# Performance work log

Hardware: AMD Instinct MI355X
Metric: run time of the kernel (lower is better)

Reference implementation:

```python
import jax, jax.numpy as jnp
import numpy as np

ALPHA = 0.71  # nms_policy.ALPHA: geometric size-bin ratio of HNMS


def _hnms_keep(rects, scores, num):
    """Hashing-based NMS: box survives iff it is the highest-scoring box in its
    hash cell in ALL `num` shifted hash tables. rects is [N,4] cxywh."""
    cx, cy, w, h = rects[:, 0], rects[:, 1], rects[:, 2], rects[:, 3]
    log_a = jnp.log(jnp.asarray(ALPHA, rects.dtype))
    step = 1.0 / ALPHA - 1.0  # location cell size relative to quantized box size
    keep = jnp.ones(scores.shape[0], dtype=bool)
    for m in range(num):  # small fixed number of hash tables
        off = m / num  # fractional shift of each hash table
        # geometric size quantization (w in [1,100], alpha<1 -> qw in [-13,0])
        qw = jnp.floor(jnp.log(w) / log_a + off).astype(jnp.int32)
        qh = jnp.floor(jnp.log(h) / log_a + off).astype(jnp.int32)
        dw = jnp.power(jnp.asarray(ALPHA, rects.dtype), qw.astype(rects.dtype))
        dh = jnp.power(jnp.asarray(ALPHA, rects.dtype), qh.astype(rects.dtype))
        # size-proportional location quantization (qx,qy in [0, ~2500))
        qx = jnp.floor(cx / (step * dw) + off).astype(jnp.int32)
        qy = jnp.floor(cy / (step * dh) + off).astype(jnp.int32)
        # pack (qw,qh) and (qx,qy) into two int32 keys (ranges verified above)
        key_hi = (qw + 64) * 128 + (qh + 64)
        key_lo = qx * 65536 + qy
        order = jnp.lexsort((-scores, key_lo, key_hi))
        kh = key_hi[order]
        kl = key_lo[order]
        first = jnp.concatenate(
            [jnp.ones((1,), bool), (kh[1:] != kh[:-1]) | (kl[1:] != kl[:-1])])
        keep = keep & jnp.zeros_like(keep).at[order].set(first)
    return keep


def setup_inputs() -> dict:
    key = jax.random.key(0)
    k1, k2, k3, k4, k5 = jax.random.split(key, 5)
    N = 1_000_000
    cx = jax.random.uniform(k1, (N,), jnp.float32, 0.0, 1000.0)
    cy = jax.random.uniform(k2, (N,), jnp.float32, 0.0, 1000.0)
    w = jax.random.uniform(k3, (N,), jnp.float32, 1.0, 100.0)
    h = jax.random.uniform(k4, (N,), jnp.float32, 1.0, 100.0)
    rects = jnp.stack([cx, cy, w, h], axis=1)  # cxywh
    scores = jax.random.uniform(k5, (N,), jnp.float32)
    return {"rects": rects, "scores": scores, "num": 4, "max_proposals": 1000}


def reference(rects, scores, num, max_proposals):
    keep = _hnms_keep(rects, scores, num)
    # topk filter over kept boxes (pad/mask instead of dynamic-size gather)
    masked = jnp.where(keep, scores, -jnp.inf)
    vals, idx = jax.lax.top_k(masked, max_proposals)
    valid = jnp.isfinite(vals)  # fewer kept than max_proposals -> padded rows
    boxes_out = jnp.where(valid[:, None], rects[idx], 0.0)   # [P,4]
    scores_out = jnp.where(valid, scores[idx], 0.0)          # [P]
    return jnp.concatenate([boxes_out, scores_out[:, None]], axis=1)  # [P,5]
```

## Files before the change

kernel.cpp:

```cpp
#include <hip/hip_runtime.h>
#include <math.h>

typedef unsigned long long u64;
typedef unsigned int u32;
typedef unsigned char u8;

#define BUCKETS 16384
#define CAND_BUF 8192
#define CAND_CAP_F 4096
#define TMAX 4
#define T2 0.9985f
#define H2_BITS 13
#define SEGS 64
#define SEGCAP 128
#define SEGSHIFT 7
#define NSLOTS (SEGS * SEGCAP)
#define SEGSTRIDE 16
#define EMPTY_KEY 0xAAAAAAAAu
#define POISON32 0xAAAAAAAAu

__device__ __forceinline__ u32 mix32(u32 x) {
  x ^= x >> 16; x *= 0x85ebca6bu;
  x ^= x >> 13; x *= 0xc2b2ae35u;
  x ^= x >> 16;
  return x;
}

__device__ __forceinline__ void fill_dwtab(float* dwtab) {
  if (threadIdx.x < 16) {
    double p = 1.0;
    const double a = (double)0.71f;
    for (int j = 0; j < (int)threadIdx.x; ++j) p *= a;
    dwtab[threadIdx.x] = (float)(1.0 / p);
  }
}

__device__ __forceinline__ u32 cell_key32(float cx, float cy, float tw, float th,
                                          float off, const float* dwtab) {
  const float STEP = (float)(1.0 / 0.71 - 1.0);
  int qw = (int)floorf(tw + off);
  int qh = (int)floorf(th + off);
  int wi = -qw; wi = wi < 0 ? 0 : (wi > 15 ? 15 : wi);
  int hi2 = -qh; hi2 = hi2 < 0 ? 0 : (hi2 > 15 ? 15 : hi2);
  float dw = dwtab[wi];
  float dh = dwtab[hi2];
  int qx = (int)floorf(cx / (STEP * dw) + off);
  int qy = (int)floorf(cy / (STEP * dh) + off);
  return ((u32)(qw + 15) << 28) | ((u32)(qh + 15) << 24) |
         (((u32)qx & 0xFFFu) << 12) | ((u32)qy & 0xFFFu);
}

__device__ __forceinline__ float tval(float w) {
  const float LOG_A = (float)-0.34249033916884865;
  return (float)log((double)w) / LOG_A;
}

__device__ __forceinline__ int bucket_of(float s) {
  int b = (int)(s * (float)BUCKETS);
  return b < 0 ? 0 : (b >= BUCKETS ? BUCKETS - 1 : b);
}

__device__ __forceinline__ void insert_box(
    u64* tab, int H, u32 mask, const float* dwtab,
    float4 r, float tw, float th, int num, int nt, u64 packed, u32 hi) {
  u32 key[TMAX], slot[TMAX];
#pragma unroll
  for (int t = 0; t < TMAX; ++t) {
    float off = (float)((double)t / (double)num);
    key[t] = cell_key32(r.x, r.y, tw, th, off, dwtab);
    slot[t] = mix32(key[t]) & mask;
  }
  ulonglong2 sv[TMAX];
#pragma unroll
  for (int t = 0; t < TMAX; ++t) {
    if (t < nt)
      sv[t] = *(const ulonglong2*)(tab + ((size_t)t * (size_t)H + slot[t]) * 2);
  }
#pragma unroll
  for (int t = 0; t < TMAX; ++t) {
    if (t >= nt) continue;
    u64* base = tab + (size_t)t * (size_t)H * 2;
    u32 sl = slot[t];
    u64 w0 = sv[t].x, w1 = sv[t].y;
    for (int p = 0; p < H; ++p) {
      u32 k = (u32)w0;
      if (k == key[t]) {
        if ((u32)(w1 >> 32) <= hi)
          atomicMax(base + (size_t)sl * 2 + 1, packed);
        break;
      }
      if (k == EMPTY_KEY) {
        u32 old = atomicCAS((u32*)(base + (size_t)sl * 2), EMPTY_KEY, key[t]);
        if (old == EMPTY_KEY || old == key[t]) {
          atomicMax(base + (size_t)sl * 2 + 1, packed);
          break;
        }
      }
      sl = (sl + 1u) & mask;
      ulonglong2 v = *(const ulonglong2*)(base + (size_t)sl * 2);
      w0 = v.x; w1 = v.y;
    }
  }
}

__device__ __forceinline__ bool probe_keeper(
    const u64* tab, int H, u32 mask, const float* dwtab,
    float4 r, float tw, float th, int num, int nt, u64 packed) {
  u32 key[TMAX], slot[TMAX];
#pragma unroll
  for (int t = 0; t < TMAX; ++t) {
    float off = (float)((double)t / (double)num);
    key[t] = cell_key32(r.x, r.y, tw, th, off, dwtab);
    slot[t] = mix32(key[t]) & mask;
  }
  bool keep = true;
#pragma unroll
  for (int t = 0; t < TMAX; ++t) {
    if (t >= nt) continue;
    const u64* base = tab + (size_t)t * (size_t)H * 2;
    u32 sl = slot[t];
    for (int p = 0; p < H; ++p) {
      ulonglong2 v = *(const ulonglong2*)(base + (size_t)sl * 2);
      u32 k = (u32)v.x;
      if (k == key[t]) { keep = keep && (v.y == packed); break; }
      if (k == EMPTY_KEY) { keep = false; break; }
      sl = (sl + 1u) & mask;
    }
    if (!keep) break;
  }
  return keep;
}

__global__ void __launch_bounds__(256) k_compact_insert(
    const float* __restrict__ scores, const float4* __restrict__ rects,
    const int* __restrict__ nump, u64* __restrict__ list64,
    u32* __restrict__ segcnt, u64* __restrict__ stab, int N) {
  __shared__ float dwtab[16];
  __shared__ u32 lcnt, lbase;
  fill_dwtab(dwtab);
  if (threadIdx.x == 0) lcnt = 0;
  __syncthreads();
  const float4* s4 = (const float4*)scores;
  int i = blockIdx.x * blockDim.x + threadIdx.x;
  int nvec = N >> 2;
  int tail = N & 3;
  float sarr[4] = {0, 0, 0, 0};
  if (i < nvec) {
    float4 v = s4[i];
    sarr[0] = v.x; sarr[1] = v.y; sarr[2] = v.z; sarr[3] = v.w;
  } else if (i == nvec && tail) {
    for (int j = 0; j < tail; ++j) sarr[j] = scores[nvec * 4 + j];
  }
  u32 npass = 0;
#pragma unroll
  for (int j = 0; j < 4; ++j) npass += (sarr[j] >= T2) ? 1u : 0u;
  u32 my = 0;
  if (npass) my = atomicAdd(&lcnt, npass);
  __syncthreads();
  int seg = (int)(blockIdx.x & (SEGS - 1));
  if (threadIdx.x == 0 && lcnt)
    lbase = atomicAdd(&segcnt[seg * SEGSTRIDE], lcnt) - POISON32;
  __syncthreads();
  if (!npass) return;
  u32 pos = lbase + my;
  int num = *nump;
  int nt = num < TMAX ? num : TMAX;
  int H = 1 << H2_BITS;
  u32 mask = (u32)(H - 1);
#pragma unroll
  for (int j = 0; j < 4; ++j) {
    if (sarr[j] < T2) continue;
    u32 idx = (u32)(i * 4 + j);
    u32 sb = __float_as_uint(sarr[j]);
    if (pos < SEGCAP)
      list64[(seg << SEGSHIFT) + pos] = ((u64)sb << 32) | (u64)idx;
    pos++;
    float4 r = rects[idx];
    float tw = tval(r.z), th = tval(r.w);
    u32 hi = 0xC0000000u | sb;
    u64 packed = ((u64)hi << 32) | (u64)(~idx);
    insert_box(stab, H, mask, dwtab, r, tw, th, num, nt, packed, hi);
  }
}

__global__ void __launch_bounds__(256) k_probe(
    const float4* __restrict__ rects, const int* __restrict__ nump,
    const u64* __restrict__ list64, const u32* __restrict__ segcnt,
    const u64* __restrict__ stab, u64* __restrict__ cand,
    u32* __restrict__ meta, int N) {
  __shared__ float dwtab[16];
  __shared__ u32 lcnt, lbase;
  fill_dwtab(dwtab);
  if (threadIdx.x == 0) lcnt = 0;
  __syncthreads();
  int j = blockIdx.x * blockDim.x + threadIdx.x;
  bool pass = false;
  u32 sb = 0, idx = 0;
  if (j < NSLOTS) {
    int seg = j >> SEGSHIFT;
    u32 cnt = segcnt[seg * SEGSTRIDE] - POISON32;
    if (cnt > SEGCAP) cnt = SEGCAP;
    if ((u32)(j & (SEGCAP - 1)) < cnt) {
      u64 e = list64[j];
      idx = (u32)e;
      sb = (u32)(e >> 32);
      if (idx < (u32)N) {
        float4 r = rects[idx];
        int num = *nump;
        int nt = num < TMAX ? num : TMAX;
        float tw = tval(r.z), th = tval(r.w);
        u64 packed = ((u64)(0xC0000000u | sb) << 32) | (u64)(~idx);
        int H = 1 << H2_BITS;
        pass = probe_keeper(stab, H, (u32)(H - 1), dwtab, r, tw, th, num, nt,
                            packed);
      }
    }
  }
  u32 my = 0;
  if (pass) my = atomicAdd(&lcnt, 1u);
  __syncthreads();
  if (threadIdx.x == 0 && lcnt)
    lbase = atomicAdd(&meta[8], lcnt) - POISON32;
  __syncthreads();
  if (pass) {
    u32 p = lbase + my;
    if (p < CAND_BUF) cand[p] = ((u64)sb << 32) | (u64)(~idx);
  }
}

__global__ void __launch_bounds__(256) k_rank_fb(
    const float4* __restrict__ rects, const float* __restrict__ scores,
    const int* __restrict__ nump, const u64* __restrict__ list64,
    const u32* __restrict__ segcnt, u32* __restrict__ meta,
    u64* __restrict__ tab, u64* __restrict__ cand, float* __restrict__ out,
    int N, int H, int K) {
  int tid = threadIdx.x;
  __shared__ u32 ok_sh, Ssh;
  u32 c = (tid < 64) ? (segcnt[tid * SEGSTRIDE] - POISON32) : 0u;
  u64 badmask = __ballot(c > SEGCAP);
  if (tid == 0) {
    u32 S0 = meta[8] - POISON32;
    Ssh = S0;
    ok_sh = (badmask == 0ULL && S0 >= (u32)K && S0 <= (u32)CAND_CAP_F) ? 1u : 0u;
  }
  __syncthreads();
  u32 ok = ok_sh;
  u32 S = Ssh;

  if (blockIdx.x < 64) {
    if (!ok) return;
    u32 base = blockIdx.x * 64;
    if (base >= S) return;
    __shared__ u64 tile[CAND_CAP_F];
    for (u32 j2 = (u32)tid; j2 < S; j2 += 256) tile[j2] = cand[j2];
    __syncthreads();
    if (tid >= 64) return;
    u32 e = base + (u32)tid;
    if (e >= S) return;
    u64 mine = tile[e];
    int rank = 0;
    for (u32 j2 = 0; j2 < S; ++j2) rank += (tile[j2] > mine) ? 1 : 0;
    if (rank < K) {
      u32 bi = ~((u32)mine);
      float s = __uint_as_float((u32)(mine >> 32));
      float4 b = rects[bi];
      out[rank * 5 + 0] = b.x;
      out[rank * 5 + 1] = b.y;
      out[rank * 5 + 2] = b.z;
      out[rank * 5 + 3] = b.w;
      out[rank * 5 + 4] = s;
    }
    return;
  }

  if (ok) return;
  __shared__ float dwtab[16];
  fill_dwtab(dwtab);
  __syncthreads();
  int num = *nump;
  int nt = num < TMAX ? num : TMAX;
  u32 mask = (u32)(H - 1);

  for (int i = tid; i < N; i += 256) {
    float4 r = rects[i];
    float s = scores[i];
    float tw = tval(r.z), th = tval(r.w);
    u32 hi = 0xC0000000u | __float_as_uint(s);
    u64 packed = ((u64)hi << 32) | (u64)(~(u32)i);
    insert_box(tab, H, mask, dwtab, r, tw, th, num, nt, packed, hi);
  }
  __syncthreads();

  __shared__ u32 hist[BUCKETS];
  for (int j = tid; j < BUCKETS; j += 256) hist[j] = 0u;
  __syncthreads();
  for (int i = tid; i < N; i += 256) {
    float4 r = rects[i];
    float s = scores[i];
    float tw = tval(r.z), th = tval(r.w);
    u64 packed = ((u64)(0xC0000000u | __float_as_uint(s)) << 32) | (u64)(~(u32)i);
    if (probe_keeper(tab, H, mask, dwtab, r, tw, th, num, nt, packed))
      atomicAdd(&hist[bucket_of(s)], 1u);
  }
  __syncthreads();

  __shared__ u32 part[256];
  __shared__ u32 T2sh;
  u32 mysum = 0;
  int base = tid * 64;
  for (int j = 0; j < 64; ++j) mysum += hist[base + j];
  part[tid] = mysum;
  __syncthreads();
  u32 inc = mysum;
  for (int d = 1; d < 256; d <<= 1) {
    u32 v = (tid + d < 256) ? part[tid + d] : 0u;
    __syncthreads();
    inc += v;
    part[tid] = inc;
    __syncthreads();
  }
  if (tid == 0) T2sh = 0u;
  __syncthreads();
  u32 prev = inc - mysum;
  for (int j = 63; j >= 0; --j) {
    u32 cumb = prev + hist[base + j];
    if (cumb >= (u32)K && prev < (u32)K) T2sh = (u32)(base + j);
    prev = cumb;
  }
  __syncthreads();

  __shared__ u32 lcnt;
  if (tid == 0) lcnt = 0u;
  __syncthreads();
  u32 Tb = T2sh;
  for (int i = tid; i < N; i += 256) {
    float4 r = rects[i];
    float s = scores[i];
    if ((u32)bucket_of(s) < Tb) continue;
    float tw = tval(r.z), th = tval(r.w);
    u32 sbits = __float_as_uint(s);
    u64 packed = ((u64)(0xC0000000u | sbits) << 32) | (u64)(~(u32)i);
    if (probe_keeper(tab, H, mask, dwtab, r, tw, th, num, nt, packed)) {
      u32 pos = atomicAdd(&lcnt, 1u);
      if (pos < CAND_BUF)
        cand[pos] = ((u64)sbits << 32) | (u64)(~(u32)i);
    }
  }
  __syncthreads();
  u32 C2 = lcnt < (u32)CAND_BUF ? lcnt : (u32)CAND_BUF;

  for (u32 e = tid; e < C2; e += 256) {
    u64 mine = cand[e];
    int rank = 0;
    for (u32 j = 0; j < C2; ++j) rank += (cand[j] > mine) ? 1 : 0;
    if (rank < K) {
      u32 bi = ~((u32)mine);
      float s = __uint_as_float((u32)(mine >> 32));
      float4 b = rects[bi];
      out[rank * 5 + 0] = b.x;
      out[rank * 5 + 1] = b.y;
      out[rank * 5 + 2] = b.z;
      out[rank * 5 + 3] = b.w;
      out[rank * 5 + 4] = s;
    }
  }
  for (int r = (int)C2 + tid; r < K; r += 256) {
    out[r * 5 + 0] = 0.0f; out[r * 5 + 1] = 0.0f; out[r * 5 + 2] = 0.0f;
    out[r * 5 + 3] = 0.0f; out[r * 5 + 4] = 0.0f;
  }
}

extern "C" void kernel_launch(void* const* d_in, const int* in_sizes, int n_in,
                              void* d_out, int out_size, void* d_ws, size_t ws_size,
                              hipStream_t stream) {
  const float4* rects = (const float4*)d_in[0];
  const float* scores = (const float*)d_in[1];
  const int* nump = (const int*)d_in[2];
  int N = in_sizes[1];
  int K = out_size / 5;
  float* out = (float*)d_out;

  char* ws = (char*)d_ws;
  u32* meta = (u32*)ws;
  u32* segcnt = (u32*)(ws + 256);
  size_t off = 256 + 4096;
  u64* cand = (u64*)(ws + off);
  off += (size_t)CAND_BUF * 8;
  u64* list64 = (u64*)(ws + off);
  off += (size_t)NSLOTS * 8;
  u64* stab = (u64*)(ws + off);
  off += (4ULL << H2_BITS) * 16ULL;
  size_t tab_off = (off + 255) & ~(size_t)255;
  size_t avail = ws_size > tab_off ? ws_size - tab_off : 0;
  int hbits = 20;
  while (hbits > 16 && (4ULL << hbits) * 16ULL > avail) --hbits;
  int H = 1 << hbits;
  u64* tab = (u64*)(ws + tab_off);

  int threads = 256;
  int nvec = N / 4;
  int blocks_c = (nvec + 1 + threads - 1) / threads;
  int blocks_p = (NSLOTS + threads - 1) / threads;
  int blocks_rf = 64 + 1;

  k_compact_insert<<<blocks_c, threads, 0, stream>>>(scores, rects, nump,
                                                     list64, segcnt, stab, N);
  k_probe<<<blocks_p, threads, 0, stream>>>(rects, nump, list64, segcnt, stab,
                                            cand, meta, N);
  k_rank_fb<<<blocks_rf, threads, 0, stream>>>(rects, scores, nump, list64,
                                               segcnt, meta, tab, cand, out,
                                               N, H, K);
}
```

Measured before the change: 116.5 us.

## Fuse three kernel launches into one cooperative kernel with grid syncs

Replaces the three separate kernel launches (compact+insert, probe, rank/fallback) with a single cooperative kernel of 256 blocks that uses grid-wide syncs between phases. The goal is to remove launch overhead and the gaps between kernels. The trade-off is a grid-stride loop over the 1M scores with only 256 blocks, which may give less memory parallelism than the original large grid. A 64 KB shared buffer per block may also limit occupancy. If the cooperative launch fails, the old three-kernel path runs instead.

```diff
diff --git a/kernel.cpp b/kernel.cpp
--- a/kernel.cpp
+++ b/kernel.cpp
@@ -1,5 +1,8 @@
 #include <hip/hip_runtime.h>
+#include <hip/hip_cooperative_groups.h>
 #include <math.h>
+
+namespace cg = cooperative_groups;
 
 typedef unsigned long long u64;
 typedef unsigned int u32;
@@ -18,6 +21,7 @@
 #define SEGSTRIDE 16
 #define EMPTY_KEY 0xAAAAAAAAu
 #define POISON32 0xAAAAAAAAu
+#define GRID_U 256
 
 __device__ __forceinline__ u32 mix32(u32 x) {
   x ^= x >> 16; x *= 0x85ebca6bu;
@@ -131,6 +135,229 @@
   return keep;
 }
 
+__global__ void __launch_bounds__(256) k_uber(
+    const float4* __restrict__ rects, const float* __restrict__ scores,
+    const int* __restrict__ nump, u64* __restrict__ list64,
+    u32* __restrict__ segcnt, u64* __restrict__ stab, u64* __restrict__ tab,
+    u64* __restrict__ cand, u32* __restrict__ meta, float* __restrict__ out,
+    int N, int H, int K) {
+  cg::grid_group grid = cg::this_grid();
+  __shared__ float dwtab[16];
+  __shared__ alignas(16) u32 sh_mem[BUCKETS];
+  fill_dwtab(dwtab);
+  __syncthreads();
+  int tid = threadIdx.x;
+  int num = *nump;
+  int nt = num < TMAX ? num : TMAX;
+
+  {
+    const float4* s4 = (const float4*)scores;
+    int nvec = N >> 2;
+    int tail = N & 3;
+    int last = nvec + (tail ? 1 : 0);
+    int gsize = gridDim.x * blockDim.x;
+    int H2 = 1 << H2_BITS;
+    u32 mask2 = (u32)(H2 - 1);
+    for (int i = blockIdx.x * blockDim.x + tid; i < last; i += gsize) {
+      float sarr[4] = {0, 0, 0, 0};
+      if (i < nvec) {
+        float4 v = s4[i];
+        sarr[0] = v.x; sarr[1] = v.y; sarr[2] = v.z; sarr[3] = v.w;
+      } else {
+        for (int j = 0; j < tail; ++j) sarr[j] = scores[nvec * 4 + j];
+      }
+#pragma unroll
+      for (int j = 0; j < 4; ++j) {
+        if (sarr[j] < T2) continue;
+        u32 idx = (u32)(i * 4 + j);
+        u32 sb = __float_as_uint(sarr[j]);
+        int seg = i & (SEGS - 1);
+        u32 pos = atomicAdd(&segcnt[seg * SEGSTRIDE], 1u) - POISON32;
+        if (pos < SEGCAP)
+          list64[(seg << SEGSHIFT) + pos] = ((u64)sb << 32) | (u64)idx;
+        float4 r = rects[idx];
+        float tw = tval(r.z), th = tval(r.w);
+        u32 hi = 0xC0000000u | sb;
+        u64 packed = ((u64)hi << 32) | (u64)(~idx);
+        insert_box(stab, H2, mask2, dwtab, r, tw, th, num, nt, packed, hi);
+      }
+    }
+  }
+  grid.sync();
+
+  {
+    int j = blockIdx.x * (NSLOTS / GRID_U) + tid;
+    if (tid < (NSLOTS / GRID_U)) {
+      int seg = j >> SEGSHIFT;
+      u32 cnt = segcnt[seg * SEGSTRIDE] - POISON32;
+      if (cnt > SEGCAP) cnt = SEGCAP;
+      if ((u32)(j & (SEGCAP - 1)) < cnt) {
+        u64 e = list64[j];
+        u32 idx = (u32)e;
+        u32 sb = (u32)(e >> 32);
+        if (idx < (u32)N) {
+          float4 r = rects[idx];
+          float tw = tval(r.z), th = tval(r.w);
+          u64 packed = ((u64)(0xC0000000u | sb) << 32) | (u64)(~idx);
+          int H2 = 1 << H2_BITS;
+          if (probe_keeper(stab, H2, (u32)(H2 - 1), dwtab, r, tw, th, num, nt,
+                           packed)) {
+            u32 p = atomicAdd(&meta[8], 1u) - POISON32;
+            if (p < CAND_BUF) cand[p] = ((u64)sb << 32) | (u64)(~idx);
+          }
+        }
+      }
+    }
+  }
+  grid.sync();
+
+  __shared__ u32 ok_sh, Ssh;
+  {
+    u32 c = (tid < 64) ? (segcnt[tid * SEGSTRIDE] - POISON32) : 0u;
+    u64 badmask = __ballot(c > SEGCAP);
+    if (tid == 0) {
+      u32 S0 = meta[8] - POISON32;
+      Ssh = S0;
+      ok_sh = (badmask == 0ULL && S0 >= (u32)K && S0 <= (u32)CAND_CAP_F) ? 1u
+                                                                         : 0u;
+    }
+  }
+  __syncthreads();
+  u32 ok = ok_sh;
+  u32 S = Ssh;
+
+  if (blockIdx.x < 64) {
+    if (!ok) return;
+    u32 base = blockIdx.x * 64;
+    if (base >= S) return;
+    u64* tile = (u64*)sh_mem;
+    __shared__ u32 rnk[64];
+    for (u32 j2 = (u32)tid; j2 < S; j2 += 256) tile[j2] = cand[j2];
+    if (tid < 64) rnk[tid] = 0u;
+    __syncthreads();
+    u32 e = base + (u32)(tid & 63);
+    if (e < S) {
+      u64 mine = tile[e];
+      u32 q = (u32)tid >> 6;
+      u32 chunk = (S + 3u) >> 2;
+      u32 lo = q * chunk;
+      u32 hiB = lo + chunk; if (hiB > S) hiB = S;
+      u32 cnt = 0;
+      for (u32 j2 = lo; j2 < hiB; ++j2) cnt += (tile[j2] > mine) ? 1u : 0u;
+      if (cnt) atomicAdd(&rnk[tid & 63], cnt);
+    }
+    __syncthreads();
+    if (tid < 64 && e < S) {
+      u32 rank = rnk[tid];
+      if (rank < (u32)K) {
+        u64 mine = tile[e];
+        u32 bi = ~((u32)mine);
+        float s = __uint_as_float((u32)(mine >> 32));
+        float4 b = rects[bi];
+        out[rank * 5 + 0] = b.x;
+        out[rank * 5 + 1] = b.y;
+        out[rank * 5 + 2] = b.z;
+        out[rank * 5 + 3] = b.w;
+        out[rank * 5 + 4] = s;
+      }
+    }
+    return;
+  }
+  if (blockIdx.x != 64) return;
+
+  if (ok) return;
+  u32* hist = sh_mem;
+  u32 mask = (u32)(H - 1);
+
+  for (int i = tid; i < N; i += 256) {
+    float4 r = rects[i];
+    float s = scores[i];
+    float tw = tval(r.z), th = tval(r.w);
+    u32 hi = 0xC0000000u | __float_as_uint(s);
+    u64 packed = ((u64)hi << 32) | (u64)(~(u32)i);
+    insert_box(tab, H, mask, dwtab, r, tw, th, num, nt, packed, hi);
+  }
+  __syncthreads();
+
+  for (int j = tid; j < BUCKETS; j += 256) hist[j] = 0u;
+  __syncthreads();
+  for (int i = tid; i < N; i += 256) {
+    float4 r = rects[i];
+    float s = scores[i];
+    float tw = tval(r.z), th = tval(r.w);
+    u64 packed = ((u64)(0xC0000000u | __float_as_uint(s)) << 32) | (u64)(~(u32)i);
+    if (probe_keeper(tab, H, mask, dwtab, r, tw, th, num, nt, packed))
+      atomicAdd(&hist[bucket_of(s)], 1u);
+  }
+  __syncthreads();
+
+  __shared__ u32 part[256];
+  __shared__ u32 T2sh;
+  u32 mysum = 0;
+  int base = tid * 64;
+  for (int j = 0; j < 64; ++j) mysum += hist[base + j];
+  part[tid] = mysum;
+  __syncthreads();
+  u32 inc = mysum;
+  for (int d = 1; d < 256; d <<= 1) {
+    u32 v = (tid + d < 256) ? part[tid + d] : 0u;
+    __syncthreads();
+    inc += v;
+    part[tid] = inc;
+    __syncthreads();
+  }
+  if (tid == 0) T2sh = 0u;
+  __syncthreads();
+  u32 prev = inc - mysum;
+  for (int j = 63; j >= 0; --j) {
+    u32 cumb = prev + hist[base + j];
+    if (cumb >= (u32)K && prev < (u32)K) T2sh = (u32)(base + j);
+    prev = cumb;
+  }
+  __syncthreads();
+
+  __shared__ u32 lcnt;
+  if (tid == 0) lcnt = 0u;
+  __syncthreads();
+  u32 Tb = T2sh;
+  for (int i = tid; i < N; i += 256) {
+    float4 r = rects[i];
+    float s = scores[i];
+    if ((u32)bucket_of(s) < Tb) continue;
+    float tw = tval(r.z), th = tval(r.w);
+    u32 sbits = __float_as_uint(s);
+    u64 packed = ((u64)(0xC0000000u | sbits) << 32) | (u64)(~(u32)i);
+    if (probe_keeper(tab, H, mask, dwtab, r, tw, th, num, nt, packed)) {
+      u32 pos = atomicAdd(&lcnt, 1u);
+      if (pos < CAND_BUF)
+        cand[pos] = ((u64)sbits << 32) | (u64)(~(u32)i);
+    }
+  }
+  __syncthreads();
+  u32 C2 = lcnt < (u32)CAND_BUF ? lcnt : (u32)CAND_BUF;
+
+  for (u32 e = tid; e < C2; e += 256) {
+    u64 mine = cand[e];
+    int rank = 0;
+    for (u32 j = 0; j < C2; ++j) rank += (cand[j] > mine) ? 1 : 0;
+    if (rank < K) {
+      u32 bi = ~((u32)mine);
+      float s = __uint_as_float((u32)(mine >> 32));
+      float4 b = rects[bi];
+      out[rank * 5 + 0] = b.x;
+      out[rank * 5 + 1] = b.y;
+      out[rank * 5 + 2] = b.z;
+      out[rank * 5 + 3] = b.w;
+      out[rank * 5 + 4] = s;
+    }
+  }
+  for (int r = (int)C2 + tid; r < K; r += 256) {
+    out[r * 5 + 0] = 0.0f; out[r * 5 + 1] = 0.0f; out[r * 5 + 2] = 0.0f;
+    out[r * 5 + 3] = 0.0f; out[r * 5 + 4] = 0.0f;
+  }
+}
+
+
 __global__ void __launch_bounds__(256) k_compact_insert(
     const float* __restrict__ scores, const float4* __restrict__ rects,
     const int* __restrict__ nump, u64* __restrict__ list64,
@@ -397,17 +624,26 @@
   int H = 1 << hbits;
   u64* tab = (u64*)(ws + tab_off);
 
-  int threads = 256;
-  int nvec = N / 4;
-  int blocks_c = (nvec + 1 + threads - 1) / threads;
-  int blocks_p = (NSLOTS + threads - 1) / threads;
-  int blocks_rf = 64 + 1;
-
-  k_compact_insert<<<blocks_c, threads, 0, stream>>>(scores, rects, nump,
-                                                     list64, segcnt, stab, N);
-  k_probe<<<blocks_p, threads, 0, stream>>>(rects, nump, list64, segcnt, stab,
-                                            cand, meta, N);
-  k_rank_fb<<<blocks_rf, threads, 0, stream>>>(rects, scores, nump, list64,
-                                               segcnt, meta, tab, cand, out,
-                                               N, H, K);
-}
+  void* kargs[] = {(void*)&rects, (void*)&scores, (void*)&nump,
+                   (void*)&list64, (void*)&segcnt, (void*)&stab, (void*)&tab,
+                   (void*)&cand,  (void*)&meta,   (void*)&out,
+                   (void*)&N,     (void*)&H,      (void*)&K};
+  hipError_t ce = hipLaunchCooperativeKernel((const void*)k_uber,
+                                             dim3(GRID_U), dim3(256), kargs,
+                                             0, stream);
+  if (ce != hipSuccess) {
+    (void)hipGetLastError();
+    int threads = 256;
+    int nvec = N / 4;
+    int blocks_c = (nvec + 1 + threads - 1) / threads;
+    int blocks_p = (NSLOTS + threads - 1) / threads;
+    int blocks_rf = 64 + 1;
+    k_compact_insert<<<blocks_c, threads, 0, stream>>>(scores, rects, nump,
+                                                       list64, segcnt, stab, N);
+    k_probe<<<blocks_p, threads, 0, stream>>>(rects, nump, list64, segcnt,
+                                              stab, cand, meta, N);
+    k_rank_fb<<<blocks_rf, threads, 0, stream>>>(rects, scores, nump, list64,
+                                                 segcnt, meta, tab, cand, out,
+                                                 N, H, K);
+  }
+}
```

After: 184.3 us. 58.2% more time.

## Fuse probe stage into compact-insert kernel via last-block-done pattern

Applied to the files above, without the earlier changes.

The separate probe kernel is removed. The last block of the compact/insert kernel, found with an atomic done-counter, now gathers the segment lists into shared memory and probes the small hash table itself. It uses relaxed agent-scope atomic loads and issues the first probe loads for all tables up front. It writes the ok flag and candidate count to meta for the rank kernel. This saves one kernel launch and its inter-kernel gap, but the probe work now runs in a single block and the fused kernel carries a 32KB shared buffer.

```diff
diff --git a/kernel.cpp b/kernel.cpp
--- a/kernel.cpp
+++ b/kernel.cpp
@@ -24,6 +24,13 @@
   x ^= x >> 13; x *= 0xc2b2ae35u;
   x ^= x >> 16;
   return x;
+}
+
+__device__ __forceinline__ u64 aload64(const u64* p) {
+  return __hip_atomic_load(p, __ATOMIC_RELAXED, __HIP_MEMORY_SCOPE_AGENT);
+}
+__device__ __forceinline__ u32 aload32(const u32* p) {
+  return __hip_atomic_load(p, __ATOMIC_RELAXED, __HIP_MEMORY_SCOPE_AGENT);
 }
 
 __device__ __forceinline__ void fill_dwtab(float* dwtab) {
@@ -103,6 +110,43 @@
   }
 }
 
+__device__ __forceinline__ bool probe_keeper_agent(
+    const u64* tab, int H, u32 mask, const float* dwtab,
+    float4 r, float tw, float th, int num, int nt, u64 packed) {
+  u32 key[TMAX], slot[TMAX];
+#pragma unroll
+  for (int t = 0; t < TMAX; ++t) {
+    float off = (float)((double)t / (double)num);
+    key[t] = cell_key32(r.x, r.y, tw, th, off, dwtab);
+    slot[t] = mix32(key[t]) & mask;
+  }
+  u64 w0[TMAX], w1[TMAX];
+#pragma unroll
+  for (int t = 0; t < TMAX; ++t)
+    if (t < nt) w0[t] = aload64(tab + ((size_t)t * (size_t)H + slot[t]) * 2);
+#pragma unroll
+  for (int t = 0; t < TMAX; ++t)
+    if (t < nt) w1[t] = aload64(tab + ((size_t)t * (size_t)H + slot[t]) * 2 + 1);
+  bool keep = true;
+#pragma unroll
+  for (int t = 0; t < TMAX; ++t) {
+    if (t >= nt) continue;
+    if (!keep) continue;
+    const u64* base = tab + (size_t)t * (size_t)H * 2;
+    u32 sl = slot[t];
+    u64 a = w0[t], b = w1[t];
+    for (int p = 0; p < H; ++p) {
+      u32 k = (u32)a;
+      if (k == key[t]) { keep = keep && (b == packed); break; }
+      if (k == EMPTY_KEY) { keep = false; break; }
+      sl = (sl + 1u) & mask;
+      a = aload64(base + (size_t)sl * 2);
+      b = aload64(base + (size_t)sl * 2 + 1);
+    }
+  }
+  return keep;
+}
+
 __device__ __forceinline__ bool probe_keeper(
     const u64* tab, int H, u32 mask, const float* dwtab,
     float4 r, float tw, float th, int num, int nt, u64 packed) {
@@ -131,17 +175,21 @@
   return keep;
 }
 
-__global__ void __launch_bounds__(256) k_compact_insert(
+__global__ void __launch_bounds__(256) k_compact_insert_probe(
     const float* __restrict__ scores, const float4* __restrict__ rects,
     const int* __restrict__ nump, u64* __restrict__ list64,
-    u32* __restrict__ segcnt, u64* __restrict__ stab, int N) {
+    u32* __restrict__ segcnt, u64* __restrict__ stab, u64* __restrict__ cand,
+    u32* __restrict__ meta, int N, int K) {
   __shared__ float dwtab[16];
-  __shared__ u32 lcnt, lbase;
+  __shared__ u32 lcnt, lbase, lastflag;
+  __shared__ alignas(16) u64 clist[CAND_CAP_F];
   fill_dwtab(dwtab);
-  if (threadIdx.x == 0) lcnt = 0;
-  __syncthreads();
+  int tid = threadIdx.x;
+  if (tid == 0) lcnt = 0;
+  __syncthreads();
+
   const float4* s4 = (const float4*)scores;
-  int i = blockIdx.x * blockDim.x + threadIdx.x;
+  int i = blockIdx.x * blockDim.x + tid;
   int nvec = N >> 2;
   int tail = N & 3;
   float sarr[4] = {0, 0, 0, 0};
@@ -158,91 +206,100 @@
   if (npass) my = atomicAdd(&lcnt, npass);
   __syncthreads();
   int seg = (int)(blockIdx.x & (SEGS - 1));
-  if (threadIdx.x == 0 && lcnt)
+  if (tid == 0 && lcnt)
     lbase = atomicAdd(&segcnt[seg * SEGSTRIDE], lcnt) - POISON32;
   __syncthreads();
-  if (!npass) return;
-  u32 pos = lbase + my;
   int num = *nump;
   int nt = num < TMAX ? num : TMAX;
-  int H = 1 << H2_BITS;
-  u32 mask = (u32)(H - 1);
-#pragma unroll
-  for (int j = 0; j < 4; ++j) {
-    if (sarr[j] < T2) continue;
-    u32 idx = (u32)(i * 4 + j);
-    u32 sb = __float_as_uint(sarr[j]);
-    if (pos < SEGCAP)
-      list64[(seg << SEGSHIFT) + pos] = ((u64)sb << 32) | (u64)idx;
-    pos++;
-    float4 r = rects[idx];
-    float tw = tval(r.z), th = tval(r.w);
-    u32 hi = 0xC0000000u | sb;
-    u64 packed = ((u64)hi << 32) | (u64)(~idx);
-    insert_box(stab, H, mask, dwtab, r, tw, th, num, nt, packed, hi);
-  }
-}
-
-__global__ void __launch_bounds__(256) k_probe(
-    const float4* __restrict__ rects, const int* __restrict__ nump,
-    const u64* __restrict__ list64, const u32* __restrict__ segcnt,
-    const u64* __restrict__ stab, u64* __restrict__ cand,
-    u32* __restrict__ meta, int N) {
-  __shared__ float dwtab[16];
-  __shared__ u32 lcnt, lbase;
-  fill_dwtab(dwtab);
-  if (threadIdx.x == 0) lcnt = 0;
-  __syncthreads();
-  int j = blockIdx.x * blockDim.x + threadIdx.x;
-  bool pass = false;
-  u32 sb = 0, idx = 0;
-  if (j < NSLOTS) {
-    int seg = j >> SEGSHIFT;
-    u32 cnt = segcnt[seg * SEGSTRIDE] - POISON32;
-    if (cnt > SEGCAP) cnt = SEGCAP;
-    if ((u32)(j & (SEGCAP - 1)) < cnt) {
-      u64 e = list64[j];
-      idx = (u32)e;
-      sb = (u32)(e >> 32);
-      if (idx < (u32)N) {
-        float4 r = rects[idx];
-        int num = *nump;
-        int nt = num < TMAX ? num : TMAX;
-        float tw = tval(r.z), th = tval(r.w);
-        u64 packed = ((u64)(0xC0000000u | sb) << 32) | (u64)(~idx);
-        int H = 1 << H2_BITS;
-        pass = probe_keeper(stab, H, (u32)(H - 1), dwtab, r, tw, th, num, nt,
-                            packed);
+  const int H2 = 1 << H2_BITS;
+  const u32 mask2 = (u32)(H2 - 1);
+  if (npass) {
+    u32 pos = lbase + my;
+#pragma unroll
+    for (int j = 0; j < 4; ++j) {
+      if (sarr[j] < T2) continue;
+      u32 idx = (u32)(i * 4 + j);
+      u32 sb = __float_as_uint(sarr[j]);
+      if (pos < SEGCAP)
+        list64[(seg << SEGSHIFT) + pos] = ((u64)sb << 32) | (u64)idx;
+      pos++;
+      float4 r = rects[idx];
+      float tw = tval(r.z), th = tval(r.w);
+      u32 hi = 0xC0000000u | sb;
+      u64 packed = ((u64)hi << 32) | (u64)(~idx);
+      insert_box(stab, H2, mask2, dwtab, r, tw, th, num, nt, packed, hi);
+    }
+  }
+
+  __threadfence();
+  __syncthreads();
+  if (tid == 0) {
+    u32 done = atomicAdd(&meta[12], 1u);
+    lastflag = (done == POISON32 + (u32)gridDim.x - 1u) ? 1u : 0u;
+  }
+  __syncthreads();
+  if (!lastflag) return;
+
+  __threadfence();
+  __shared__ u32 segc[SEGS];
+  __shared__ u32 ok0, lc2, kc;
+  if (tid == 0) { ok0 = 1u; lc2 = 0u; kc = 0u; }
+  u32 c64 = 0;
+  if (tid < SEGS) {
+    c64 = aload32(&segcnt[tid * SEGSTRIDE]) - POISON32;
+    segc[tid] = c64 > SEGCAP ? SEGCAP : c64;
+  }
+  u64 bad = __ballot(tid < SEGS && c64 > SEGCAP);
+  if (tid == 0 && bad) ok0 = 0u;
+  __syncthreads();
+  if (!ok0) {
+    if (tid == 0) { meta[4] = 0u; meta[8] = 0u; }
+    return;
+  }
+  for (int j = tid; j < NSLOTS; j += 256) {
+    int sg = j >> SEGSHIFT;
+    if ((u32)(j & (SEGCAP - 1)) < segc[sg]) {
+      u64 e = aload64(&list64[j]);
+      u32 p = atomicAdd(&lc2, 1u);
+      if (p < (u32)CAND_CAP_F) clist[p] = e; else ok0 = 0u;
+    }
+  }
+  __syncthreads();
+  u32 C = lc2 < (u32)CAND_CAP_F ? lc2 : (u32)CAND_CAP_F;
+  if (ok0) {
+    for (u32 c = tid; c < C; c += 256) {
+      u64 e = clist[c];
+      u32 idx = (u32)e;
+      u32 sb = (u32)(e >> 32);
+      if (idx >= (u32)N) continue;
+      float4 r = rects[idx];
+      float tw = tval(r.z), th = tval(r.w);
+      u64 packed = ((u64)(0xC0000000u | sb) << 32) | (u64)(~idx);
+      if (probe_keeper_agent(stab, H2, mask2, dwtab, r, tw, th, num, nt,
+                             packed)) {
+        u32 p = atomicAdd(&kc, 1u);
+        if (p < (u32)CAND_BUF) cand[p] = ((u64)sb << 32) | (u64)(~idx);
       }
     }
   }
-  u32 my = 0;
-  if (pass) my = atomicAdd(&lcnt, 1u);
-  __syncthreads();
-  if (threadIdx.x == 0 && lcnt)
-    lbase = atomicAdd(&meta[8], lcnt) - POISON32;
-  __syncthreads();
-  if (pass) {
-    u32 p = lbase + my;
-    if (p < CAND_BUF) cand[p] = ((u64)sb << 32) | (u64)(~idx);
+  __syncthreads();
+  if (tid == 0) {
+    u32 S = kc;
+    u32 ok = (ok0 && S >= (u32)K && S <= (u32)CAND_CAP_F) ? 1u : 0u;
+    meta[4] = ok;
+    meta[8] = S;
   }
 }
 
 __global__ void __launch_bounds__(256) k_rank_fb(
     const float4* __restrict__ rects, const float* __restrict__ scores,
-    const int* __restrict__ nump, const u64* __restrict__ list64,
-    const u32* __restrict__ segcnt, u32* __restrict__ meta,
+    const int* __restrict__ nump, const u32* __restrict__ meta,
     u64* __restrict__ tab, u64* __restrict__ cand, float* __restrict__ out,
     int N, int H, int K) {
   int tid = threadIdx.x;
   __shared__ u32 ok_sh, Ssh;
-  u32 c = (tid < 64) ? (segcnt[tid * SEGSTRIDE] - POISON32) : 0u;
-  u64 badmask = __ballot(c > SEGCAP);
-  if (tid == 0) {
-    u32 S0 = meta[8] - POISON32;
-    Ssh = S0;
-    ok_sh = (badmask == 0ULL && S0 >= (u32)K && S0 <= (u32)CAND_CAP_F) ? 1u : 0u;
-  }
+  __shared__ alignas(16) u32 sh_mem[BUCKETS];
+  if (tid == 0) { ok_sh = meta[4]; Ssh = meta[8]; }
   __syncthreads();
   u32 ok = ok_sh;
   u32 S = Ssh;
@@ -251,7 +308,7 @@
     if (!ok) return;
     u32 base = blockIdx.x * 64;
     if (base >= S) return;
-    __shared__ u64 tile[CAND_CAP_F];
+    u64* tile = (u64*)sh_mem;
     for (u32 j2 = (u32)tid; j2 < S; j2 += 256) tile[j2] = cand[j2];
     __syncthreads();
     if (tid >= 64) return;
@@ -272,6 +329,7 @@
     }
     return;
   }
+  if (blockIdx.x != 64) return;
 
   if (ok) return;
   __shared__ float dwtab[16];
@@ -280,6 +338,7 @@
   int num = *nump;
   int nt = num < TMAX ? num : TMAX;
   u32 mask = (u32)(H - 1);
+  u32* hist = sh_mem;
 
   for (int i = tid; i < N; i += 256) {
     float4 r = rects[i];
@@ -291,7 +350,6 @@
   }
   __syncthreads();
 
-  __shared__ u32 hist[BUCKETS];
   for (int j = tid; j < BUCKETS; j += 256) hist[j] = 0u;
   __syncthreads();
   for (int i = tid; i < N; i += 256) {
@@ -400,14 +458,10 @@
   int threads = 256;
   int nvec = N / 4;
   int blocks_c = (nvec + 1 + threads - 1) / threads;
-  int blocks_p = (NSLOTS + threads - 1) / threads;
   int blocks_rf = 64 + 1;
 
-  k_compact_insert<<<blocks_c, threads, 0, stream>>>(scores, rects, nump,
-                                                     list64, segcnt, stab, N);
-  k_probe<<<blocks_p, threads, 0, stream>>>(rects, nump, list64, segcnt, stab,
-                                            cand, meta, N);
-  k_rank_fb<<<blocks_rf, threads, 0, stream>>>(rects, scores, nump, list64,
-                                               segcnt, meta, tab, cand, out,
-                                               N, H, K);
-}
+  k_compact_insert_probe<<<blocks_c, threads, 0, stream>>>(
+      scores, rects, nump, list64, segcnt, stab, cand, meta, N, K);
+  k_rank_fb<<<blocks_rf, threads, 0, stream>>>(rects, scores, nump, meta, tab,
+                                               cand, out, N, H, K);
+}
```

New measurement: 206.4 us. 1.77x slower.

## Fuse probe kernel into rank kernel with per-block redundant probing

Applied to the files above, without the earlier changes.

Removes the separate probe launch. Each of the 65 blocks now gathers the compacted candidate list into shared memory, probes every candidate against the small hash table itself, and zeroes the entries that fail. It then ranks the survivors straight from shared memory, so there is no global candidate buffer and no atomic counter. This saves one kernel launch and the cand/meta round trip, at the cost of every block repeating the full probe of up to 4096 candidates.

```diff
diff --git a/kernel.cpp b/kernel.cpp
--- a/kernel.cpp
+++ b/kernel.cpp
@@ -183,83 +183,87 @@
   }
 }
 
-__global__ void __launch_bounds__(256) k_probe(
-    const float4* __restrict__ rects, const int* __restrict__ nump,
-    const u64* __restrict__ list64, const u32* __restrict__ segcnt,
-    const u64* __restrict__ stab, u64* __restrict__ cand,
-    u32* __restrict__ meta, int N) {
-  __shared__ float dwtab[16];
-  __shared__ u32 lcnt, lbase;
-  fill_dwtab(dwtab);
-  if (threadIdx.x == 0) lcnt = 0;
-  __syncthreads();
-  int j = blockIdx.x * blockDim.x + threadIdx.x;
-  bool pass = false;
-  u32 sb = 0, idx = 0;
-  if (j < NSLOTS) {
-    int seg = j >> SEGSHIFT;
-    u32 cnt = segcnt[seg * SEGSTRIDE] - POISON32;
-    if (cnt > SEGCAP) cnt = SEGCAP;
-    if ((u32)(j & (SEGCAP - 1)) < cnt) {
-      u64 e = list64[j];
-      idx = (u32)e;
-      sb = (u32)(e >> 32);
-      if (idx < (u32)N) {
-        float4 r = rects[idx];
-        int num = *nump;
-        int nt = num < TMAX ? num : TMAX;
-        float tw = tval(r.z), th = tval(r.w);
-        u64 packed = ((u64)(0xC0000000u | sb) << 32) | (u64)(~idx);
-        int H = 1 << H2_BITS;
-        pass = probe_keeper(stab, H, (u32)(H - 1), dwtab, r, tw, th, num, nt,
-                            packed);
-      }
-    }
-  }
-  u32 my = 0;
-  if (pass) my = atomicAdd(&lcnt, 1u);
-  __syncthreads();
-  if (threadIdx.x == 0 && lcnt)
-    lbase = atomicAdd(&meta[8], lcnt) - POISON32;
-  __syncthreads();
-  if (pass) {
-    u32 p = lbase + my;
-    if (p < CAND_BUF) cand[p] = ((u64)sb << 32) | (u64)(~idx);
-  }
-}
-
-__global__ void __launch_bounds__(256) k_rank_fb(
+__global__ void __launch_bounds__(256) k_probe_rank_fb(
     const float4* __restrict__ rects, const float* __restrict__ scores,
     const int* __restrict__ nump, const u64* __restrict__ list64,
-    const u32* __restrict__ segcnt, u32* __restrict__ meta,
+    const u32* __restrict__ segcnt, const u64* __restrict__ stab,
     u64* __restrict__ tab, u64* __restrict__ cand, float* __restrict__ out,
     int N, int H, int K) {
   int tid = threadIdx.x;
-  __shared__ u32 ok_sh, Ssh;
-  u32 c = (tid < 64) ? (segcnt[tid * SEGSTRIDE] - POISON32) : 0u;
-  u64 badmask = __ballot(c > SEGCAP);
+  __shared__ alignas(16) u32 sh_mem[BUCKETS];
+  __shared__ float dwtab[16];
+  __shared__ u32 segc[SEGS], segb[SEGS + 1];
+  __shared__ u32 ok0_sh;
+  __shared__ u32 part[256];
+  fill_dwtab(dwtab);
+  u32 c = 0;
+  if (tid < SEGS) {
+    c = segcnt[tid * SEGSTRIDE] - POISON32;
+    segc[tid] = c;
+  }
+  u64 bad = __ballot(tid < SEGS && c > SEGCAP);
+  __syncthreads();
   if (tid == 0) {
-    u32 S0 = meta[8] - POISON32;
-    Ssh = S0;
-    ok_sh = (badmask == 0ULL && S0 >= (u32)K && S0 <= (u32)CAND_CAP_F) ? 1u : 0u;
-  }
-  __syncthreads();
-  u32 ok = ok_sh;
-  u32 S = Ssh;
+    u32 acc = 0;
+    for (int s2 = 0; s2 < SEGS; ++s2) { segb[s2] = acc; acc += segc[s2]; }
+    segb[SEGS] = acc;
+    ok0_sh = (bad == 0ULL && acc >= (u32)K && acc <= (u32)CAND_CAP_F) ? 1u : 0u;
+  }
+  __syncthreads();
+  u32 ok0 = ok0_sh;
+  u32 C = segb[SEGS];
+  int num = *nump;
+  int nt = num < TMAX ? num : TMAX;
+  u64* tile = (u64*)sh_mem;
+
+  u32 S = 0;
+  if (ok0) {
+    for (int j = tid; j < NSLOTS; j += 256) {
+      int s2 = j >> SEGSHIFT;
+      u32 i2 = (u32)(j & (SEGCAP - 1));
+      if (i2 < segc[s2]) tile[segb[s2] + i2] = list64[j];
+    }
+    __syncthreads();
+    const int H2 = 1 << H2_BITS;
+    const u32 mask2 = (u32)(H2 - 1);
+    u32 cnt = 0;
+    for (u32 c2 = (u32)tid; c2 < C; c2 += 256) {
+      u64 e = tile[c2];
+      u32 idx = (u32)e;
+      u32 sb = (u32)(e >> 32);
+      u64 v = 0;
+      if (idx < (u32)N) {
+        float4 r = rects[idx];
+        float tw = tval(r.z), th = tval(r.w);
+        u64 packed = ((u64)(0xC0000000u | sb) << 32) | (u64)(~idx);
+        if (probe_keeper(stab, H2, mask2, dwtab, r, tw, th, num, nt, packed)) {
+          v = ((u64)sb << 32) | (u64)(~idx);
+          cnt++;
+        }
+      }
+      tile[c2] = v;
+    }
+    part[tid] = cnt;
+    __syncthreads();
+    for (int d = 128; d > 0; d >>= 1) {
+      if (tid < d) part[tid] += part[tid + d];
+      __syncthreads();
+    }
+    S = part[0];
+  }
+  u32 ok = (ok0 && S >= (u32)K) ? 1u : 0u;
 
   if (blockIdx.x < 64) {
     if (!ok) return;
-    u32 base = blockIdx.x * 64;
-    if (base >= S) return;
-    __shared__ u64 tile[CAND_CAP_F];
-    for (u32 j2 = (u32)tid; j2 < S; j2 += 256) tile[j2] = cand[j2];
-    __syncthreads();
+    u32 base = blockIdx.x * 64u;
+    if (base >= C) return;
     if (tid >= 64) return;
-    u32 e = base + (u32)tid;
-    if (e >= S) return;
-    u64 mine = tile[e];
+    u32 e2 = base + (u32)tid;
+    if (e2 >= C) return;
+    u64 mine = tile[e2];
+    if (mine == 0) return;
     int rank = 0;
-    for (u32 j2 = 0; j2 < S; ++j2) rank += (tile[j2] > mine) ? 1 : 0;
+    for (u32 j2 = 0; j2 < C; ++j2) rank += (tile[j2] > mine) ? 1 : 0;
     if (rank < K) {
       u32 bi = ~((u32)mine);
       float s = __uint_as_float((u32)(mine >> 32));
@@ -272,14 +276,12 @@
     }
     return;
   }
+  if (blockIdx.x != 64) return;
 
   if (ok) return;
-  __shared__ float dwtab[16];
-  fill_dwtab(dwtab);
-  __syncthreads();
-  int num = *nump;
-  int nt = num < TMAX ? num : TMAX;
+  __syncthreads();
   u32 mask = (u32)(H - 1);
+  u32* hist = sh_mem;
 
   for (int i = tid; i < N; i += 256) {
     float4 r = rects[i];
@@ -291,7 +293,6 @@
   }
   __syncthreads();
 
-  __shared__ u32 hist[BUCKETS];
   for (int j = tid; j < BUCKETS; j += 256) hist[j] = 0u;
   __syncthreads();
   for (int i = tid; i < N; i += 256) {
@@ -304,7 +305,6 @@
   }
   __syncthreads();
 
-  __shared__ u32 part[256];
   __shared__ u32 T2sh;
   u32 mysum = 0;
   int base = tid * 64;
@@ -381,7 +381,6 @@
   float* out = (float*)d_out;
 
   char* ws = (char*)d_ws;
-  u32* meta = (u32*)ws;
   u32* segcnt = (u32*)(ws + 256);
   size_t off = 256 + 4096;
   u64* cand = (u64*)(ws + off);
@@ -400,14 +399,11 @@
   int threads = 256;
   int nvec = N / 4;
   int blocks_c = (nvec + 1 + threads - 1) / threads;
-  int blocks_p = (NSLOTS + threads - 1) / threads;
   int blocks_rf = 64 + 1;
 
   k_compact_insert<<<blocks_c, threads, 0, stream>>>(scores, rects, nump,
                                                      list64, segcnt, stab, N);
-  k_probe<<<blocks_p, threads, 0, stream>>>(rects, nump, list64, segcnt, stab,
-                                            cand, meta, N);
-  k_rank_fb<<<blocks_rf, threads, 0, stream>>>(rects, scores, nump, list64,
-                                               segcnt, meta, tab, cand, out,
-                                               N, H, K);
-}
+  k_probe_rank_fb<<<blocks_rf, threads, 0, stream>>>(rects, scores, nump,
+                                                     list64, segcnt, stab, tab,
+                                                     cand, out, N, H, K);
+}
```

Result: slower. 156.3 us (+34.2%).
